# Kernel optimization log

Measured on AMD Instinct MI355X. Metric: run time of the kernel, lower is better.

The kernel has to match this reference:

```python
import math
import jax, jax.numpy as jnp
import numpy as np

D = 768
H = 12
P = 128  # sup_bdist
L = 512
B = 8
DH = D // H
EPS = 1e-5


def _ln(x, w, b):
    mu = jnp.mean(x, axis=-1, keepdims=True)
    var = jnp.mean(jnp.square(x - mu), axis=-1, keepdims=True)
    return (x - mu) * jax.lax.rsqrt(var + EPS) * w + b


def setup_inputs() -> dict:
    key = jax.random.key(0)
    ks = jax.random.split(key, 16)
    s_in = 1.0 / math.sqrt(D)
    s_ff = 1.0 / math.sqrt(4 * D)
    return {
        "x": jax.random.normal(ks[0], (L, B, D), jnp.float32),
        "edge": jax.random.normal(ks[1], (B * H, L, L), jnp.float32) * 0.1,
        "bdist": jax.random.randint(ks[2], (L, L, B), 0, P),
        "W_in": jax.random.uniform(ks[3], (3 * D, D), jnp.float32, -s_in, s_in),
        "b_in": jax.random.uniform(ks[4], (3 * D,), jnp.float32, -s_in, s_in),
        "pe_emb": jax.random.normal(ks[5], (P, D), jnp.float32),
        "W_out": jax.random.uniform(ks[6], (D, D), jnp.float32, -s_in, s_in),
        "b_out": jax.random.uniform(ks[7], (D,), jnp.float32, -s_in, s_in),
        "W1": jax.random.uniform(ks[8], (4 * D, D), jnp.float32, -s_in, s_in),
        "b1": jax.random.uniform(ks[9], (4 * D,), jnp.float32, -s_in, s_in),
        "W2": jax.random.uniform(ks[10], (D, 4 * D), jnp.float32, -s_ff, s_ff),
        "b2": jax.random.uniform(ks[11], (D,), jnp.float32, -s_ff, s_ff),
        "ln1_w": jnp.ones((D,), jnp.float32),
        "ln1_b": jnp.zeros((D,), jnp.float32),
        "ln2_w": jnp.ones((D,), jnp.float32),
        "ln2_b": jnp.zeros((D,), jnp.float32),
    }


def reference(x, edge, bdist, W_in, b_in, pe_emb, W_out, b_out,
              W1, b1, W2, b2, ln1_w, ln1_b, ln2_w, ln2_b):
    # x: [L,B,D], edge: [B*H,L,L], bdist: [L,L,B]
    x_res = x
    xn = _ln(x, ln1_w, ln1_b)
    qkv = xn @ W_in.T + b_in                      # [L,B,3D]
    q, k, v = jnp.split(qkv, 3, axis=-1)
    # -> [B,H,L,Dh]
    def to_bhld(t):
        return t.reshape(L, B, H, DH).transpose(1, 2, 0, 3)
    q, k, v = to_bhld(q), to_bhld(k), to_bhld(v)

    t = jnp.einsum('bhid,bhjd->bhij', q, k)      # QK^T

    # relative-position embeddings projected through the shared in_proj
    pe_proj = pe_emb @ W_in.T + b_in             # [P,3D]
    pe_q = pe_proj[:, :D].reshape(P, H, DH)
    pe_k = pe_proj[:, D:2 * D].reshape(P, H, DH)

    # pe_t_k[b,h,i,j] = <peq(bdist[i,j,b]), k[b,h,j]>;  pe_t_q analogous with q,pek
    kp = jnp.einsum('bhjd,phd->bhjp', k, pe_q)   # [B,H,L,P]
    qp = jnp.einsum('bhid,phd->bhip', q, pe_k)   # [B,H,L,P]
    idx = jnp.transpose(bdist, (2, 0, 1))        # [B,L,L]
    j_idx = jnp.arange(L)[None, :]               # broadcast over rows i
    i_idx = jnp.arange(L)[:, None]               # broadcast over cols j
    pe_t_k = jax.vmap(lambda kp_b, id_b: kp_b[:, j_idx, id_b])(kp, idx)  # [B,H,L,L]
    pe_t_q = jax.vmap(lambda qp_b, id_b: qp_b[:, i_idx, id_b])(qp, idx)  # [B,H,L,L]

    t = t + pe_t_k + pe_t_q
    dedge = t                                    # unscaled scores (no edge bias)
    inv = 1.0 / math.sqrt(DH)
    scores = t * inv + edge.reshape(B, H, L, L)
    attn = jax.nn.softmax(scores, axis=-1)
    o = jnp.einsum('bhij,bhjd->bhid', attn, v)   # [B,H,L,Dh]
    o = o.transpose(2, 0, 1, 3).reshape(L, B, D)
    o = o @ W_out.T + b_out

    x1 = x_res + o
    h = _ln(x1, ln2_w, ln2_b)
    ff = jax.nn.gelu(h @ W1.T + b1, approximate=False) @ W2.T + b2
    x_out = x1 + ff

    edge_out = edge + (dedge * inv).reshape(B * H, L, L)
    return x_out, edge_out
```

## Files before the change

### kernel.cpp

```cpp
#include <hip/hip_runtime.h>
#include <hip/hip_bf16.h>
#include <math.h>

#define LL 512
#define BB 8
#define DD 768
#define HH 12
#define DHH 64
#define PP 128

typedef unsigned char u8;
typedef unsigned short u16;
typedef unsigned int u32;
typedef __attribute__((ext_vector_type(8))) short bf16x8;
typedef __attribute__((ext_vector_type(4))) float f32x4;

__device__ __forceinline__ u16 f2bf(float f) {
  u32 u = __float_as_uint(f);
  u32 r = (u + 0x7fffu + ((u >> 16) & 1u)) >> 16;
  return (u16)r;
}
__device__ __forceinline__ float bf2f(u32 u) {
  return __uint_as_float((u & 0xffffu) << 16);
}

#define GLDS(g, l)                                                             \
  __builtin_amdgcn_global_load_lds(                                            \
      (const __attribute__((address_space(1))) void*)(g),                      \
      (__attribute__((address_space(3))) void*)(l), 16, 0, 0)

__device__ __forceinline__ void block_reduce2(float& a, float& b, float* sbuf) {
#pragma unroll
  for (int off = 32; off > 0; off >>= 1) {
    a += __shfl_down(a, off, 64);
    b += __shfl_down(b, off, 64);
  }
  int wid = threadIdx.x >> 6, lane = threadIdx.x & 63;
  __syncthreads();
  if (lane == 0) { sbuf[wid] = a; sbuf[4 + wid] = b; }
  __syncthreads();
  a = sbuf[0] + sbuf[1] + sbuf[2] + sbuf[3];
  b = sbuf[4] + sbuf[5] + sbuf[6] + sbuf[7];
}

__global__ __launch_bounds__(256) void prep_kernel(
    const float* __restrict__ x, const float* __restrict__ ln1w,
    const float* __restrict__ ln1b, u16* __restrict__ xnb,
    const float* __restrict__ W_in, u16* __restrict__ W_inb,
    const float* __restrict__ W_out, u16* __restrict__ W_outb,
    const float* __restrict__ W1, u16* __restrict__ W1b,
    const float* __restrict__ W2, u16* __restrict__ W2b,
    const float* __restrict__ pe_emb, u16* __restrict__ peemb,
    const int* __restrict__ bdist, u8* __restrict__ bdT) {
  int blk = blockIdx.x;
  int t = threadIdx.x;
  if (blk < 4096) {
    __shared__ float sbuf[8];
    const float* xr = x + (size_t)blk * DD;
    float v0 = xr[t], v1 = xr[t + 256], v2 = xr[t + 512];
    float s = v0 + v1 + v2;
    float ss = v0 * v0 + v1 * v1 + v2 * v2;
    block_reduce2(s, ss, sbuf);
    float mu = s * (1.0f / DD);
    float var = ss * (1.0f / DD) - mu * mu;
    float r = rsqrtf(var + 1e-5f);
    u16* orow = xnb + (size_t)blk * DD;
    orow[t]       = f2bf((v0 - mu) * r * ln1w[t]       + ln1b[t]);
    orow[t + 256] = f2bf((v1 - mu) * r * ln1w[t + 256] + ln1b[t + 256]);
    orow[t + 512] = f2bf((v2 - mu) * r * ln1w[t + 512] + ln1b[t + 512]);
  } else if (blk < 11008) {
    int idx = (blk - 4096) * 256 + t;
    const float* in;
    u16* out;
    if (idx < 442368) { in = W_in; out = W_inb; }
    else if (idx < 589824) { in = W_out; out = W_outb; idx -= 442368; }
    else if (idx < 1179648) { in = W1; out = W1b; idx -= 589824; }
    else { in = W2; out = W2b; idx -= 1179648; }
    float4 v = *(const float4*)(in + (size_t)idx * 4);
    u32 lo = (u32)f2bf(v.x) | ((u32)f2bf(v.y) << 16);
    u32 hi = (u32)f2bf(v.z) | ((u32)f2bf(v.w) << 16);
    *(uint2*)(out + (size_t)idx * 4) = make_uint2(lo, hi);
  } else if (blk < 11104) {
    int idx = (blk - 11008) * 256 + t;
    float4 v = *(const float4*)(pe_emb + (size_t)idx * 4);
    u32 lo = (u32)f2bf(v.x) | ((u32)f2bf(v.y) << 16);
    u32 hi = (u32)f2bf(v.z) | ((u32)f2bf(v.w) << 16);
    *(uint2*)(peemb + (size_t)idx * 4) = make_uint2(lo, hi);
  } else {
    int i = (blk - 11104) * 256 + t;
    int b = i & 7, jj = (i >> 3) & 511, ii = i >> 12;
    bdT[((size_t)b << 18) + ((size_t)ii << 9) + jj] = (u8)bdist[i];
  }
}

template <int ACT, int OBF, int RES>
__global__ __launch_bounds__(256) void gemm_mfma(
    const u16* __restrict__ A, int lda, const u16* __restrict__ B, int ldb,
    void* __restrict__ Cv, int ldc, const float* __restrict__ bias,
    const float* __restrict__ residual, int K) {
  __shared__ __align__(16) u16 Asl[128 * 32];
  __shared__ __align__(16) u16 Bsl[128 * 32];
  int t = threadIdx.x;
  int m0 = blockIdx.y * 128, n0 = blockIdx.x * 128;
  int lane = t & 63, w = t >> 6;
  int wr = w >> 1, wc = w & 1;
  int lr = lane & 15, lg = lane >> 4;

  f32x4 acc[4][4] = {};

  const u16* Ag0 = A + (size_t)(m0 + (t >> 2)) * lda + (t & 3) * 8;
  const u16* Ag1 = A + (size_t)(m0 + 64 + (t >> 2)) * lda + (t & 3) * 8;
  const u16* Bg0 = B + (size_t)(n0 + (t >> 2)) * ldb + (t & 3) * 8;
  const u16* Bg1 = B + (size_t)(n0 + 64 + (t >> 2)) * ldb + (t & 3) * 8;
  u16* Ad0 = &Asl[t * 8];
  u16* Ad1 = &Asl[2048 + t * 8];
  u16* Bd0 = &Bsl[t * 8];
  u16* Bd1 = &Bsl[2048 + t * 8];

  for (int k0 = 0; k0 < K; k0 += 32) {
    GLDS(Ag0 + k0, Ad0);
    GLDS(Ag1 + k0, Ad1);
    GLDS(Bg0 + k0, Bd0);
    GLDS(Bg1 + k0, Bd1);
    __syncthreads();
    bf16x8 a[4], b[4];
#pragma unroll
    for (int i = 0; i < 4; i++)
      a[i] = *(const bf16x8*)&Asl[(wr * 64 + i * 16 + lr) * 32 + lg * 8];
#pragma unroll
    for (int j = 0; j < 4; j++)
      b[j] = *(const bf16x8*)&Bsl[(wc * 64 + j * 16 + lr) * 32 + lg * 8];
#pragma unroll
    for (int i = 0; i < 4; i++)
#pragma unroll
      for (int j = 0; j < 4; j++)
        asm volatile("v_mfma_f32_16x16x32_bf16 %0, %1, %2, %0"
                     : "+v"(acc[i][j])
                     : "v"(a[i]), "v"(b[j]));
    __syncthreads();
  }
  asm volatile("s_nop 7\n\ts_nop 7" ::);

  float* Cf = (float*)Cv;
  u16* Cb = (u16*)Cv;
#pragma unroll
  for (int i = 0; i < 4; i++) {
#pragma unroll
    for (int r = 0; r < 4; r++) {
      int row = m0 + wr * 64 + i * 16 + lg * 4 + r;
#pragma unroll
      for (int j = 0; j < 4; j++) {
        int col = n0 + wc * 64 + j * 16 + lr;
        float vv = acc[i][j][r];
        if (bias) vv += bias[col];
        if (ACT) vv = 0.5f * vv * (1.0f + erff(vv * 0.70710678118654752f));
        if (RES) vv += residual[(size_t)row * ldc + col];
        if (OBF) Cb[(size_t)row * ldc + col] = f2bf(vv);
        else     Cf[(size_t)row * ldc + col] = vv;
      }
    }
  }
}

__global__ __launch_bounds__(256) void gemm_mfma_qkv(
    const u16* __restrict__ xnb, const u16* __restrict__ peemb,
    const u16* __restrict__ B, const float* __restrict__ bias,
    u16* __restrict__ qb, u16* __restrict__ kb, u16* __restrict__ vbT,
    u16* __restrict__ peb) {
  __shared__ __align__(16) u16 Asl[128 * 32];
  __shared__ __align__(16) u16 Bsl[128 * 32];
  const int lda = DD, ldb = DD, K = DD;
  int t = threadIdx.x;
  int isPE = (blockIdx.y == 32);
  const u16* A = isPE ? peemb : xnb;
  int m0 = isPE ? 0 : blockIdx.y * 128;
  int n0 = blockIdx.x * 128;
  int lane = t & 63, w = t >> 6;
  int wr = w >> 1, wc = w & 1;
  int lr = lane & 15, lg = lane >> 4;

  f32x4 acc[4][4] = {};

  const u16* Ag0 = A + (size_t)(m0 + (t >> 2)) * lda + (t & 3) * 8;
  const u16* Ag1 = A + (size_t)(m0 + 64 + (t >> 2)) * lda + (t & 3) * 8;
  const u16* Bg0 = B + (size_t)(n0 + (t >> 2)) * ldb + (t & 3) * 8;
  const u16* Bg1 = B + (size_t)(n0 + 64 + (t >> 2)) * ldb + (t & 3) * 8;
  u16* Ad0 = &Asl[t * 8];
  u16* Ad1 = &Asl[2048 + t * 8];
  u16* Bd0 = &Bsl[t * 8];
  u16* Bd1 = &Bsl[2048 + t * 8];

  for (int k0 = 0; k0 < K; k0 += 32) {
    GLDS(Ag0 + k0, Ad0);
    GLDS(Ag1 + k0, Ad1);
    GLDS(Bg0 + k0, Bd0);
    GLDS(Bg1 + k0, Bd1);
    __syncthreads();
    bf16x8 a[4], b[4];
#pragma unroll
    for (int i = 0; i < 4; i++)
      a[i] = *(const bf16x8*)&Asl[(wr * 64 + i * 16 + lr) * 32 + lg * 8];
#pragma unroll
    for (int j = 0; j < 4; j++)
      b[j] = *(const bf16x8*)&Bsl[(wc * 64 + j * 16 + lr) * 32 + lg * 8];
#pragma unroll
    for (int i = 0; i < 4; i++)
#pragma unroll
      for (int j = 0; j < 4; j++)
        asm volatile("v_mfma_f32_16x16x32_bf16 %0, %1, %2, %0"
                     : "+v"(acc[i][j])
                     : "v"(a[i]), "v"(b[j]));
    __syncthreads();
  }
  asm volatile("s_nop 7\n\ts_nop 7" ::);

#pragma unroll
  for (int i = 0; i < 4; i++) {
#pragma unroll
    for (int r = 0; r < 4; r++) {
      int row = m0 + wr * 64 + i * 16 + lg * 4 + r;
      int l = row >> 3, b = row & 7;
#pragma unroll
      for (int j = 0; j < 4; j++) {
        int col = n0 + wc * 64 + j * 16 + lr;
        u16 vv = f2bf(acc[i][j][r] + bias[col]);
        if (isPE) {
          peb[(size_t)row * (3 * DD) + col] = vv;
        } else {
          int which = col / DD, hd = col - which * DD;
          int h = hd >> 6, d = hd & 63;
          if (which == 0) {
            qb[(((size_t)(b * HH + h)) * LL + l) * DHH + d] = vv;
          } else if (which == 1) {
            kb[(((size_t)(b * HH + h)) * LL + l) * DHH + d] = vv;
          } else {
            vbT[(((size_t)(b * HH + h)) * DHH + d) * LL + l] = vv;
          }
        }
      }
    }
  }
}

__global__ __launch_bounds__(256) void attn_k64(
    const u16* __restrict__ qb, const u16* __restrict__ kb,
    const u16* __restrict__ peb, u16* __restrict__ kpb,
    u16* __restrict__ qpb, u16* __restrict__ tb) {
  __shared__ __align__(16) u16 Asl[128 * 32];
  __shared__ __align__(16) u16 Bsl[128 * 32];
  int id = blockIdx.x;
  const u16 *A, *B;
  u16* Cb;
  int lda, ldb, ldc, m0, n0;
  if (id < 768) {
    int my = id & 3, z = id >> 2;
    int sel = z / 96, zz = z - sel * 96;
    A = (sel ? qb : kb) + (size_t)zz * (LL * DHH);
    B = peb + sel * DD + (size_t)(zz % HH) * 64;
    Cb = (sel ? qpb : kpb) + (size_t)zz * (LL * PP);
    lda = DHH; ldb = 3 * DD; ldc = PP; m0 = my * 128; n0 = 0;
  } else {
    int id2 = id - 768;
    int jx = id2 & 3, my = (id2 >> 2) & 3, bh = id2 >> 4;
    A = qb + (size_t)bh * (LL * DHH);
    B = kb + (size_t)bh * (LL * DHH);
    Cb = tb + (size_t)bh * (LL * LL);
    lda = DHH; ldb = DHH; ldc = LL; m0 = my * 128; n0 = jx * 128;
  }
  int t = threadIdx.x;
  int lane = t & 63, w = t >> 6;
  int wr = w >> 1, wc = w & 1;
  int lr = lane & 15, lg = lane >> 4;

  f32x4 acc[4][4] = {};

  const u16* Ag0 = A + (size_t)(m0 + (t >> 2)) * lda + (t & 3) * 8;
  const u16* Ag1 = A + (size_t)(m0 + 64 + (t >> 2)) * lda + (t & 3) * 8;
  const u16* Bg0 = B + (size_t)(n0 + (t >> 2)) * ldb + (t & 3) * 8;
  const u16* Bg1 = B + (size_t)(n0 + 64 + (t >> 2)) * ldb + (t & 3) * 8;
  u16* Ad0 = &Asl[t * 8];
  u16* Ad1 = &Asl[2048 + t * 8];
  u16* Bd0 = &Bsl[t * 8];
  u16* Bd1 = &Bsl[2048 + t * 8];

  for (int k0 = 0; k0 < DHH; k0 += 32) {
    GLDS(Ag0 + k0, Ad0);
    GLDS(Ag1 + k0, Ad1);
    GLDS(Bg0 + k0, Bd0);
    GLDS(Bg1 + k0, Bd1);
    __syncthreads();
    bf16x8 a[4], b[4];
#pragma unroll
    for (int i = 0; i < 4; i++)
      a[i] = *(const bf16x8*)&Asl[(wr * 64 + i * 16 + lr) * 32 + lg * 8];
#pragma unroll
    for (int j = 0; j < 4; j++)
      b[j] = *(const bf16x8*)&Bsl[(wc * 64 + j * 16 + lr) * 32 + lg * 8];
#pragma unroll
    for (int i = 0; i < 4; i++)
#pragma unroll
      for (int j = 0; j < 4; j++)
        asm volatile("v_mfma_f32_16x16x32_bf16 %0, %1, %2, %0"
                     : "+v"(acc[i][j])
                     : "v"(a[i]), "v"(b[j]));
    __syncthreads();
  }
  asm volatile("s_nop 7\n\ts_nop 7" ::);

#pragma unroll
  for (int i = 0; i < 4; i++) {
#pragma unroll
    for (int r = 0; r < 4; r++) {
      int row = m0 + wr * 64 + i * 16 + lg * 4 + r;
#pragma unroll
      for (int j = 0; j < 4; j++) {
        int col = n0 + wc * 64 + j * 16 + lr;
        Cb[(size_t)row * ldc + col] = f2bf(acc[i][j][r] * 0.125f);
      }
    }
  }
}

__global__ __launch_bounds__(256) void gather_scale2(
    const u16* __restrict__ tb,
    const u16* __restrict__ kp, const u16* __restrict__ qp,
    const u8* __restrict__ bdT, const float* __restrict__ edge,
    float* __restrict__ eout, float* __restrict__ stats) {
  int bh = blockIdx.z, b = bh / HH;
  int i0 = blockIdx.y * 64, j0 = blockIdx.x * 64, jt = blockIdx.x;
  __shared__ __align__(16) u16 kpl[64][PP];
  __shared__ __align__(16) u16 qpl[64][PP];
  int tid = threadIdx.x;
  int tx = tid & 15, ty = tid >> 4;

  const u16* kpg = kp + (size_t)bh * (LL * PP);
  const u16* qpg = qp + (size_t)bh * (LL * PP);
  u16* kflat = &kpl[0][0];
  u16* qflat = &qpl[0][0];
#pragma unroll
  for (int it = 0; it < 4; it++) {
    int c = tid + it * 256;
    int row = c >> 4, ch = (c & 15) * 8;
    GLDS(&kpg[(size_t)(j0 + row) * PP + ch], &kflat[c * 8]);
    GLDS(&qpg[(size_t)(i0 + row) * PP + ch], &qflat[c * 8]);
  }
  __syncthreads();

  const u8* bd = bdT + (size_t)b * (LL * LL);
  const float* eb = edge + (size_t)bh * (LL * LL);
  const u16* tbb = tb + (size_t)bh * (LL * LL);
  float* ob = eout + (size_t)bh * (LL * LL);

  float rowm[4], rows[4];
#pragma unroll
  for (int i2 = 0; i2 < 4; i2++) {
    int row = i0 + ty * 4 + i2;
    int col0 = j0 + tx * 4;
    uchar4 p4 = *(const uchar4*)&bd[(size_t)row * LL + col0];
    float4 e4 = *(const float4*)&eb[(size_t)row * LL + col0];
    uint2 t2 = *(const uint2*)&tbb[(size_t)row * LL + col0];
    float tv[4] = {bf2f(t2.x), bf2f(t2.x >> 16), bf2f(t2.y), bf2f(t2.y >> 16)};
    int pp[4] = {p4.x, p4.y, p4.z, p4.w};
    float ee[4] = {e4.x, e4.y, e4.z, e4.w};
    float sv[4];
#pragma unroll
    for (int j2 = 0; j2 < 4; j2++) {
      float gk = bf2f((u32)kpl[tx * 4 + j2][pp[j2]]);
      float gq = bf2f((u32)qpl[ty * 4 + i2][pp[j2]]);
      sv[j2] = tv[j2] + gk + gq + ee[j2];
    }
    *(float4*)&ob[(size_t)row * LL + col0] =
        make_float4(sv[0], sv[1], sv[2], sv[3]);
    float m = fmaxf(fmaxf(sv[0], sv[1]), fmaxf(sv[2], sv[3]));
#pragma unroll
    for (int off = 1; off < 16; off <<= 1) m = fmaxf(m, __shfl_xor(m, off, 64));
    float ss = __expf(sv[0] - m) + __expf(sv[1] - m) + __expf(sv[2] - m) +
               __expf(sv[3] - m);
#pragma unroll
    for (int off = 1; off < 16; off <<= 1) ss += __shfl_xor(ss, off, 64);
    rowm[i2] = m;
    rows[i2] = ss;
  }
  if (tx == 0) {
#pragma unroll
    for (int i2 = 0; i2 < 4; i2++) {
      size_t si = ((size_t)bh * LL + i0 + ty * 4 + i2) * 16 + jt;
      stats[si] = rowm[i2];
      stats[si + 8] = rows[i2];
    }
  }
}

__global__ __launch_bounds__(256) void softmax_pv_mfma(
    const float* __restrict__ scores, const u16* __restrict__ vbT,
    const float* __restrict__ stats, u16* __restrict__ olbd) {
  int bh = blockIdx.y;
  int i0 = blockIdx.x * 64;
  int b = bh / HH, h = bh - b * HH;
  __shared__ __align__(16) u16 PL[2][64 * 32];
  __shared__ __align__(16) u16 VL[2][64 * 32];
  __shared__ float smax[64], srs[64];
  int tid = threadIdx.x;
  int tx = tid & 15, ty = tid >> 4;
  int lane = tid & 63, w = tid >> 6;
  int wr = w >> 1, wc = w & 1;
  int lr = lane & 15, lg = lane >> 4;
  const float* sbase = scores + (size_t)bh * (LL * LL);
  const u16* vt = vbT + (size_t)bh * (DHH * LL);

  if (tid < 64) {
    size_t si = ((size_t)bh * LL + i0 + tid) * 16;
    float m = stats[si];
#pragma unroll
    for (int j = 1; j < 8; j++) m = fmaxf(m, stats[si + j]);
    float s = 0.f;
#pragma unroll
    for (int j = 0; j < 8; j++) s += stats[si + 8 + j] * __expf(stats[si + j] - m);
    smax[tid] = m;
    srs[tid] = 1.0f / s;
  }
  __syncthreads();

  f32x4 acc[2][2] = {};
  int ks = tx >> 3, kk = (tx & 7) * 4;
  int vd = tid >> 2, vjo = (tid & 3) * 8;

  for (int jt = 0; jt < 8; jt++) {
    int j0 = jt * 64;
    GLDS(vt + (size_t)vd * LL + j0 + vjo, &VL[0][tid * 8]);
    GLDS(vt + (size_t)vd * LL + j0 + 32 + vjo, &VL[1][tid * 8]);
#pragma unroll
    for (int rr = 0; rr < 4; rr++) {
      int r = ty + rr * 16;
      float4 s4 = *(const float4*)(sbase + (size_t)(i0 + r) * LL + j0 + tx * 4);
      float m = smax[r], rs = srs[r];
      u16 p0 = f2bf(__expf(s4.x - m) * rs);
      u16 p1 = f2bf(__expf(s4.y - m) * rs);
      u16 p2 = f2bf(__expf(s4.z - m) * rs);
      u16 p3 = f2bf(__expf(s4.w - m) * rs);
      *(uint2*)&PL[ks][r * 32 + kk] =
          make_uint2((u32)p0 | ((u32)p1 << 16), (u32)p2 | ((u32)p3 << 16));
    }
    __syncthreads();
#pragma unroll
    for (int s2 = 0; s2 < 2; s2++) {
      bf16x8 a[2], bfr[2];
#pragma unroll
      for (int i = 0; i < 2; i++)
        a[i] = *(const bf16x8*)&PL[s2][(wr * 32 + i * 16 + lr) * 32 + lg * 8];
#pragma unroll
      for (int j = 0; j < 2; j++)
        bfr[j] = *(const bf16x8*)&VL[s2][(wc * 32 + j * 16 + lr) * 32 + lg * 8];
#pragma unroll
      for (int i = 0; i < 2; i++)
#pragma unroll
        for (int j = 0; j < 2; j++)
          asm volatile("v_mfma_f32_16x16x32_bf16 %0, %1, %2, %0"
                       : "+v"(acc[i][j])
                       : "v"(a[i]), "v"(bfr[j]));
    }
    __syncthreads();
  }
  asm volatile("s_nop 7\n\ts_nop 7" ::);

#pragma unroll
  for (int i = 0; i < 2; i++) {
#pragma unroll
    for (int r = 0; r < 4; r++) {
      int irow = i0 + wr * 32 + i * 16 + lg * 4 + r;
#pragma unroll
      for (int j = 0; j < 2; j++) {
        int d = wc * 32 + j * 16 + lr;
        olbd[((size_t)irow * BB + b) * DD + h * 64 + d] = f2bf(acc[i][j][r]);
      }
    }
  }
}

__global__ __launch_bounds__(256) void gemm_mfma_part(
    const u16* __restrict__ A, int lda, const u16* __restrict__ B, int ldb,
    u16* __restrict__ Cb, int ldc, long partStride, int Kper) {
  __shared__ __align__(16) u16 Asl[128 * 32];
  __shared__ __align__(16) u16 Bsl[128 * 32];
  int z = blockIdx.z;
  A += (size_t)z * Kper;
  B += (size_t)z * Kper;
  Cb += (size_t)z * partStride;
  int t = threadIdx.x;
  int m0 = blockIdx.y * 128, n0 = blockIdx.x * 128;
  int lane = t & 63, w = t >> 6;
  int wr = w >> 1, wc = w & 1;
  int lr = lane & 15, lg = lane >> 4;

  f32x4 acc[4][4] = {};

  const u16* Ag0 = A + (size_t)(m0 + (t >> 2)) * lda + (t & 3) * 8;
  const u16* Ag1 = A + (size_t)(m0 + 64 + (t >> 2)) * lda + (t & 3) * 8;
  const u16* Bg0 = B + (size_t)(n0 + (t >> 2)) * ldb + (t & 3) * 8;
  const u16* Bg1 = B + (size_t)(n0 + 64 + (t >> 2)) * ldb + (t & 3) * 8;
  u16* Ad0 = &Asl[t * 8];
  u16* Ad1 = &Asl[2048 + t * 8];
  u16* Bd0 = &Bsl[t * 8];
  u16* Bd1 = &Bsl[2048 + t * 8];

  for (int k0 = 0; k0 < Kper; k0 += 32) {
    GLDS(Ag0 + k0, Ad0);
    GLDS(Ag1 + k0, Ad1);
    GLDS(Bg0 + k0, Bd0);
    GLDS(Bg1 + k0, Bd1);
    __syncthreads();
    bf16x8 a[4], b[4];
#pragma unroll
    for (int i = 0; i < 4; i++)
      a[i] = *(const bf16x8*)&Asl[(wr * 64 + i * 16 + lr) * 32 + lg * 8];
#pragma unroll
    for (int j = 0; j < 4; j++)
      b[j] = *(const bf16x8*)&Bsl[(wc * 64 + j * 16 + lr) * 32 + lg * 8];
#pragma unroll
    for (int i = 0; i < 4; i++)
#pragma unroll
      for (int j = 0; j < 4; j++)
        asm volatile("v_mfma_f32_16x16x32_bf16 %0, %1, %2, %0"
                     : "+v"(acc[i][j])
                     : "v"(a[i]), "v"(b[j]));
    __syncthreads();
  }
  asm volatile("s_nop 7\n\ts_nop 7" ::);

#pragma unroll
  for (int i = 0; i < 4; i++) {
#pragma unroll
    for (int r = 0; r < 4; r++) {
      int row = m0 + wr * 64 + i * 16 + lg * 4 + r;
#pragma unroll
      for (int j = 0; j < 4; j++) {
        int col = n0 + wc * 64 + j * 16 + lr;
        Cb[(size_t)row * ldc + col] = f2bf(acc[i][j][r]);
      }
    }
  }
}

template <int NS>
__global__ __launch_bounds__(256) void combine_k(const u16* __restrict__ p,
                                                 const float* __restrict__ bias,
                                                 const float* __restrict__ res,
                                                 float* __restrict__ out) {
  int idx = blockIdx.x * 256 + threadIdx.x;
  size_t e = (size_t)idx * 4;
  uint2 pv = *(const uint2*)(p + e);
  float s0 = bf2f(pv.x), s1 = bf2f(pv.x >> 16);
  float s2 = bf2f(pv.y), s3 = bf2f(pv.y >> 16);
#pragma unroll
  for (int z = 1; z < NS; z++) {
    uint2 t2 = *(const uint2*)(p + (size_t)z * 3145728 + e);
    s0 += bf2f(t2.x); s1 += bf2f(t2.x >> 16);
    s2 += bf2f(t2.y); s3 += bf2f(t2.y >> 16);
  }
  int col = (int)(e % DD);
  float4 b4 = *(const float4*)(bias + col);
  float4 r4 = *(const float4*)(res + e);
  *(float4*)(out + e) = make_float4(s0 + b4.x + r4.x, s1 + b4.y + r4.y,
                                    s2 + b4.z + r4.z, s3 + b4.w + r4.w);
}

__global__ __launch_bounds__(256) void combine2_ln(
    const u16* __restrict__ p, const float* __restrict__ bias,
    const float* __restrict__ res, float* __restrict__ x1,
    const float* __restrict__ w, const float* __restrict__ lb,
    u16* __restrict__ xnb) {
  __shared__ float sbuf[8];
  size_t row = blockIdx.x;
  int t = threadIdx.x;
  const u16* p0 = p + row * DD;
  const u16* p1 = p + 3145728 + row * DD;
  const float* rr = res + row * DD;
  float v0 = bf2f((u32)p0[t])       + bf2f((u32)p1[t])       + bias[t]       + rr[t];
  float v1 = bf2f((u32)p0[t + 256]) + bf2f((u32)p1[t + 256]) + bias[t + 256] + rr[t + 256];
  float v2 = bf2f((u32)p0[t + 512]) + bf2f((u32)p1[t + 512]) + bias[t + 512] + rr[t + 512];
  float* xr = x1 + row * DD;
  xr[t] = v0; xr[t + 256] = v1; xr[t + 512] = v2;
  float s = v0 + v1 + v2;
  float ss = v0 * v0 + v1 * v1 + v2 * v2;
  block_reduce2(s, ss, sbuf);
  float mu = s * (1.0f / DD);
  float var = ss * (1.0f / DD) - mu * mu;
  float r = rsqrtf(var + 1e-5f);
  u16* orow = xnb + row * DD;
  orow[t]       = f2bf((v0 - mu) * r * w[t]       + lb[t]);
  orow[t + 256] = f2bf((v1 - mu) * r * w[t + 256] + lb[t + 256]);
  orow[t + 512] = f2bf((v2 - mu) * r * w[t + 512] + lb[t + 512]);
}

extern "C" void kernel_launch(void* const* d_in, const int* in_sizes, int n_in,
                              void* d_out, int out_size, void* d_ws, size_t ws_size,
                              hipStream_t stream) {
  const float* x      = (const float*)d_in[0];
  const float* edge   = (const float*)d_in[1];
  const int*   bdist  = (const int*)d_in[2];
  const float* W_in   = (const float*)d_in[3];
  const float* b_in   = (const float*)d_in[4];
  const float* pe_emb = (const float*)d_in[5];
  const float* W_out  = (const float*)d_in[6];
  const float* b_out  = (const float*)d_in[7];
  const float* W1     = (const float*)d_in[8];
  const float* b1     = (const float*)d_in[9];
  const float* W2     = (const float*)d_in[10];
  const float* b2     = (const float*)d_in[11];
  const float* ln1w   = (const float*)d_in[12];
  const float* ln1b   = (const float*)d_in[13];
  const float* ln2w   = (const float*)d_in[14];
  const float* ln2b   = (const float*)d_in[15];

  float* xout = (float*)d_out;
  float* eout = xout + (size_t)LL * BB * DD;

  float* ws = (float*)d_ws;
  u16*   xnb    = (u16*)(ws + 0);
  u16*   tb     = (u16*)(ws + 1600000);
  u16*   olbdb  = (u16*)(ws + 1600000);
  u16*   ff1b   = (u16*)(ws + 3200000);
  float* x1     = ws + 11100000;
  u16*   peemb  = (u16*)(ws + 14300000);
  u16*   part   = (u16*)(ws + 14600000);
  u16*   vbT    = (u16*)(ws + 21000000);
  float* stats  = ws + 22600000;
  u8*    bdT    = (u8*)(ws + 23400000);
  u16*   kpb    = (u16*)(ws + 24000000);
  u16*   qpb    = (u16*)(ws + 27200000);
  u16*   W1b    = (u16*)(ws + 30400000);
  u16*   W2b    = (u16*)(ws + 31600000);
  u16*   W_inb  = (u16*)(ws + 32800000);
  u16*   W_outb = (u16*)(ws + 33700000);
  u16*   qb     = (u16*)(ws + 34000000);
  u16*   kb     = (u16*)(ws + 35600000);
  u16*   peb    = (u16*)(ws + 37200000);

  prep_kernel<<<19296, 256, 0, stream>>>(x, ln1w, ln1b, xnb, W_in, W_inb,
                                         W_out, W_outb, W1, W1b, W2, W2b,
                                         pe_emb, peemb, bdist, bdT);
  gemm_mfma_qkv<<<dim3(18, 33), 256, 0, stream>>>(xnb, peemb, W_inb, b_in,
                                                  qb, kb, vbT, peb);
  attn_k64<<<2304, 256, 0, stream>>>(qb, kb, peb, kpb, qpb, tb);
  gather_scale2<<<dim3(8, 8, 96), 256, 0, stream>>>(tb, kpb, qpb, bdT, edge,
                                                    eout, stats);
  softmax_pv_mfma<<<dim3(8, 96), 256, 0, stream>>>(eout, vbT, stats, olbdb);
  gemm_mfma_part<<<dim3(6, 32, 2), 256, 0, stream>>>(
      olbdb, DD, W_outb, DD, part, DD, 3145728L, DD / 2);
  combine2_ln<<<4096, 256, 0, stream>>>(part, b_out, x, x1, ln2w, ln2b, xnb);
  gemm_mfma<1, 1, 0><<<dim3(24, 32), 256, 0, stream>>>(
      xnb, DD, W1b, DD, ff1b, 4 * DD, b1, nullptr, DD);
  gemm_mfma_part<<<dim3(6, 32, 4), 256, 0, stream>>>(
      ff1b, 4 * DD, W2b, 4 * DD, part, DD, 3145728L, DD);
  combine_k<4><<<3072, 256, 0, stream>>>(part, b2, x1, xout);
}
```

Baseline: 293.8 us.

## Loop gather kernel over all column tiles with online softmax stats

The gather/score kernel now has each block sweep all eight column tiles of a 64-row stripe, reloading the kp tile into shared memory each step and keeping running row max and sum (online softmax). It writes the final max and reciprocal sum directly, so the softmax-PV kernel no longer merges eight partial stats per row. This trades grid parallelism (768 blocks instead of 6144) and adds two barriers per tile for less stats traffic and a simpler prologue downstream.

```diff
diff --git a/kernel.cpp b/kernel.cpp
--- a/kernel.cpp
+++ b/kernel.cpp
@@ -321,13 +321,13 @@
   }
 }
 
-__global__ __launch_bounds__(256) void gather_scale2(
+__global__ __launch_bounds__(256) void gather_scale3(
     const u16* __restrict__ tb,
     const u16* __restrict__ kp, const u16* __restrict__ qp,
     const u8* __restrict__ bdT, const float* __restrict__ edge,
     float* __restrict__ eout, float* __restrict__ stats) {
-  int bh = blockIdx.z, b = bh / HH;
-  int i0 = blockIdx.y * 64, j0 = blockIdx.x * 64, jt = blockIdx.x;
+  int bh = blockIdx.y, b = bh / HH;
+  int i0 = blockIdx.x * 64;
   __shared__ __align__(16) u16 kpl[64][PP];
   __shared__ __align__(16) u16 qpl[64][PP];
   int tid = threadIdx.x;
@@ -341,8 +341,8 @@
   for (int it = 0; it < 4; it++) {
     int c = tid + it * 256;
     int row = c >> 4, ch = (c & 15) * 8;
-    GLDS(&kpg[(size_t)(j0 + row) * PP + ch], &kflat[c * 8]);
     GLDS(&qpg[(size_t)(i0 + row) * PP + ch], &qflat[c * 8]);
+    GLDS(&kpg[(size_t)row * PP + ch], &kflat[c * 8]);
   }
   __syncthreads();
 
@@ -351,42 +351,61 @@
   const u16* tbb = tb + (size_t)bh * (LL * LL);
   float* ob = eout + (size_t)bh * (LL * LL);
 
-  float rowm[4], rows[4];
-#pragma unroll
-  for (int i2 = 0; i2 < 4; i2++) {
-    int row = i0 + ty * 4 + i2;
-    int col0 = j0 + tx * 4;
-    uchar4 p4 = *(const uchar4*)&bd[(size_t)row * LL + col0];
-    float4 e4 = *(const float4*)&eb[(size_t)row * LL + col0];
-    uint2 t2 = *(const uint2*)&tbb[(size_t)row * LL + col0];
-    float tv[4] = {bf2f(t2.x), bf2f(t2.x >> 16), bf2f(t2.y), bf2f(t2.y >> 16)};
-    int pp[4] = {p4.x, p4.y, p4.z, p4.w};
-    float ee[4] = {e4.x, e4.y, e4.z, e4.w};
-    float sv[4];
-#pragma unroll
-    for (int j2 = 0; j2 < 4; j2++) {
-      float gk = bf2f((u32)kpl[tx * 4 + j2][pp[j2]]);
-      float gq = bf2f((u32)qpl[ty * 4 + i2][pp[j2]]);
-      sv[j2] = tv[j2] + gk + gq + ee[j2];
-    }
-    *(float4*)&ob[(size_t)row * LL + col0] =
-        make_float4(sv[0], sv[1], sv[2], sv[3]);
-    float m = fmaxf(fmaxf(sv[0], sv[1]), fmaxf(sv[2], sv[3]));
-#pragma unroll
-    for (int off = 1; off < 16; off <<= 1) m = fmaxf(m, __shfl_xor(m, off, 64));
-    float ss = __expf(sv[0] - m) + __expf(sv[1] - m) + __expf(sv[2] - m) +
-               __expf(sv[3] - m);
-#pragma unroll
-    for (int off = 1; off < 16; off <<= 1) ss += __shfl_xor(ss, off, 64);
-    rowm[i2] = m;
-    rows[i2] = ss;
+  float runm[4], runs[4];
+#pragma unroll
+  for (int i2 = 0; i2 < 4; i2++) { runm[i2] = -3e38f; runs[i2] = 0.f; }
+
+  for (int jt = 0; jt < 8; jt++) {
+    int j0 = jt * 64;
+#pragma unroll
+    for (int i2 = 0; i2 < 4; i2++) {
+      int row = i0 + ty * 4 + i2;
+      int col0 = j0 + tx * 4;
+      uchar4 p4 = *(const uchar4*)&bd[(size_t)row * LL + col0];
+      float4 e4 = *(const float4*)&eb[(size_t)row * LL + col0];
+      uint2 t2 = *(const uint2*)&tbb[(size_t)row * LL + col0];
+      float tv[4] = {bf2f(t2.x), bf2f(t2.x >> 16), bf2f(t2.y),
+                     bf2f(t2.y >> 16)};
+      int pp[4] = {p4.x, p4.y, p4.z, p4.w};
+      float ee[4] = {e4.x, e4.y, e4.z, e4.w};
+      float sv[4];
+#pragma unroll
+      for (int j2 = 0; j2 < 4; j2++) {
+        float gk = bf2f((u32)kpl[tx * 4 + j2][pp[j2]]);
+        float gq = bf2f((u32)qpl[ty * 4 + i2][pp[j2]]);
+        sv[j2] = tv[j2] + gk + gq + ee[j2];
+      }
+      *(float4*)&ob[(size_t)row * LL + col0] =
+          make_float4(sv[0], sv[1], sv[2], sv[3]);
+      float m = fmaxf(fmaxf(sv[0], sv[1]), fmaxf(sv[2], sv[3]));
+#pragma unroll
+      for (int off = 1; off < 16; off <<= 1)
+        m = fmaxf(m, __shfl_xor(m, off, 64));
+      float ss = __expf(sv[0] - m) + __expf(sv[1] - m) + __expf(sv[2] - m) +
+                 __expf(sv[3] - m);
+#pragma unroll
+      for (int off = 1; off < 16; off <<= 1) ss += __shfl_xor(ss, off, 64);
+      float mn = fmaxf(runm[i2], m);
+      runs[i2] = runs[i2] * __expf(runm[i2] - mn) + ss * __expf(m - mn);
+      runm[i2] = mn;
+    }
+    if (jt < 7) {
+      __syncthreads();
+#pragma unroll
+      for (int it = 0; it < 4; it++) {
+        int c = tid + it * 256;
+        int row = c >> 4, ch = (c & 15) * 8;
+        GLDS(&kpg[(size_t)((jt + 1) * 64 + row) * PP + ch], &kflat[c * 8]);
+      }
+      __syncthreads();
+    }
   }
   if (tx == 0) {
 #pragma unroll
     for (int i2 = 0; i2 < 4; i2++) {
-      size_t si = ((size_t)bh * LL + i0 + ty * 4 + i2) * 16 + jt;
-      stats[si] = rowm[i2];
-      stats[si + 8] = rows[i2];
+      size_t si = ((size_t)bh * LL + i0 + ty * 4 + i2) * 2;
+      stats[si] = runm[i2];
+      stats[si + 1] = 1.0f / runs[i2];
     }
   }
 }
@@ -409,15 +428,9 @@
   const u16* vt = vbT + (size_t)bh * (DHH * LL);
 
   if (tid < 64) {
-    size_t si = ((size_t)bh * LL + i0 + tid) * 16;
-    float m = stats[si];
-#pragma unroll
-    for (int j = 1; j < 8; j++) m = fmaxf(m, stats[si + j]);
-    float s = 0.f;
-#pragma unroll
-    for (int j = 0; j < 8; j++) s += stats[si + 8 + j] * __expf(stats[si + j] - m);
-    smax[tid] = m;
-    srs[tid] = 1.0f / s;
+    size_t si = ((size_t)bh * LL + i0 + tid) * 2;
+    smax[tid] = stats[si];
+    srs[tid] = stats[si + 1];
   }
   __syncthreads();
 
@@ -642,8 +655,8 @@
   gemm_mfma_qkv<<<dim3(18, 33), 256, 0, stream>>>(xnb, peemb, W_inb, b_in,
                                                   qb, kb, vbT, peb);
   attn_k64<<<2304, 256, 0, stream>>>(qb, kb, peb, kpb, qpb, tb);
-  gather_scale2<<<dim3(8, 8, 96), 256, 0, stream>>>(tb, kpb, qpb, bdT, edge,
-                                                    eout, stats);
+  gather_scale3<<<dim3(8, 96), 256, 0, stream>>>(tb, kpb, qpb, bdT, edge,
+                                                 eout, stats);
   softmax_pv_mfma<<<dim3(8, 96), 256, 0, stream>>>(eout, vbT, stats, olbdb);
   gemm_mfma_part<<<dim3(6, 32, 2), 256, 0, stream>>>(
       olbdb, DD, W_outb, DD, part, DD, 3145728L, DD / 2);
```

Measured after the change: 292.1 us. Within noise of the previous version (-0.6%).
